# Optimization experiments

Hardware: AMD Instinct MI355X
Metric: run time of the kernel (lower is better)

The kernel has to match this reference:

```python
import jax, jax.numpy as jnp
import numpy as np

CHUNK = 6  # SmoothLoss chunk length hard-coded in TotalLoss.forward


def setup_inputs() -> dict:
    key = jax.random.key(0)
    k1, k2, k3, k4, k5 = jax.random.split(key, 5)
    N = 3_000_000   # gru/resnet/y length, divisible by 6
    M = 500_000     # one average per 6-sample chunk
    return {
        "resnet_pred": jax.random.normal(k1, (N,), dtype=jnp.float32),
        "gru_pred": jax.random.normal(k2, (N,), dtype=jnp.float32),
        "average_pred": jax.random.normal(k3, (M,), dtype=jnp.float32),
        "y": jax.random.normal(k4, (N,), dtype=jnp.float32),
        "average_hr": jax.random.normal(k5, (M,), dtype=jnp.float32),
    }


def reference(resnet_pred, gru_pred, average_pred, y, average_hr):
    lambda_val = 100.0
    # L1 losses (mean reduction, as nn.L1Loss default)
    l1_loss = jnp.mean(jnp.abs(resnet_pred - y)) + jnp.mean(jnp.abs(average_pred - average_hr))
    # Smoothness loss: for each chunk of 6, sum_t |x_t - mean(chunk)| / 6, summed over chunks
    x = gru_pred.reshape(-1, CHUNK)                      # [C, 6]
    m = jnp.mean(x, axis=1, keepdims=True)               # [C, 1]
    smooth_loss = jnp.sum(jnp.abs(x - m)) / CHUNK        # scalar
    total_loss = l1_loss + lambda_val * smooth_loss
    return (total_loss, l1_loss, smooth_loss)
```

## Files before the change

kernel.cpp:

```cpp
#include <hip/hip_runtime.h>

#define CHUNK 6
#define BLK 256

__global__ __launch_bounds__(BLK) void loss_partial_kernel(
    const float* __restrict__ resnet, const float* __restrict__ gru,
    const float* __restrict__ avgp,   const float* __restrict__ y,
    const float* __restrict__ avgh,
    float* __restrict__ partials, int nb, int C, int M, int N)
{
    const int tid = threadIdx.x;
    const int gid = blockIdx.x * BLK + tid;
    const int T   = nb * BLK;

    float s_l1a = 0.f, s_l1b = 0.f, s_sm = 0.f;

    const int Cq = C >> 2;
    const float4* g4 = reinterpret_cast<const float4*>(gru);
    float4 q0, q1, q2, q3, q4, q5;
    const bool have_q = (gid < Cq);
    if (have_q) {
        const float4* p = g4 + 6 * gid;
        q0 = p[0]; q1 = p[1]; q2 = p[2]; q3 = p[3]; q4 = p[4]; q5 = p[5];
    }

    const int Mv4 = M >> 2;
    if (gid < Mv4) {
        float4 p = reinterpret_cast<const float4*>(avgp)[gid];
        float4 h = reinterpret_cast<const float4*>(avgh)[gid];
        s_l1b = fabsf(p.x - h.x) + fabsf(p.y - h.y)
              + fabsf(p.z - h.z) + fabsf(p.w - h.w);
    }

    const int Nv4 = N >> 2;
    const float4* r4 = reinterpret_cast<const float4*>(resnet);
    const float4* y4 = reinterpret_cast<const float4*>(y);
    for (int i = gid; i < Nv4; i += T) {
        float4 r = r4[i], v = y4[i];
        s_l1a += fabsf(r.x - v.x) + fabsf(r.y - v.y)
               + fabsf(r.z - v.z) + fabsf(r.w - v.w);
    }

    if (have_q) {
        float m0 = (q0.x + q0.y + q0.z + q0.w + q1.x + q1.y) * (1.0f / 6.0f);
        float m1 = (q1.z + q1.w + q2.x + q2.y + q2.z + q2.w) * (1.0f / 6.0f);
        float m2 = (q3.x + q3.y + q3.z + q3.w + q4.x + q4.y) * (1.0f / 6.0f);
        float m3 = (q4.z + q4.w + q5.x + q5.y + q5.z + q5.w) * (1.0f / 6.0f);
        s_sm = fabsf(q0.x-m0)+fabsf(q0.y-m0)+fabsf(q0.z-m0)+fabsf(q0.w-m0)
             + fabsf(q1.x-m0)+fabsf(q1.y-m0)
             + fabsf(q1.z-m1)+fabsf(q1.w-m1)
             + fabsf(q2.x-m1)+fabsf(q2.y-m1)+fabsf(q2.z-m1)+fabsf(q2.w-m1)
             + fabsf(q3.x-m2)+fabsf(q3.y-m2)+fabsf(q3.z-m2)+fabsf(q3.w-m2)
             + fabsf(q4.x-m2)+fabsf(q4.y-m2)
             + fabsf(q4.z-m3)+fabsf(q4.w-m3)
             + fabsf(q5.x-m3)+fabsf(q5.y-m3)+fabsf(q5.z-m3)+fabsf(q5.w-m3);
    }

    if (gid == 0) {
        for (int k = Nv4 << 2; k < N; ++k) s_l1a += fabsf(resnet[k] - y[k]);
        for (int k = Mv4 << 2; k < M; ++k) s_l1b += fabsf(avgp[k] - avgh[k]);
        for (int c = Cq << 2; c < C; ++c) {
            int base = CHUNK * c;
            float x0=gru[base],x1=gru[base+1],x2=gru[base+2];
            float x3=gru[base+3],x4=gru[base+4],x5=gru[base+5];
            float m = (x0+x1+x2+x3+x4+x5) * (1.0f/6.0f);
            s_sm += fabsf(x0-m)+fabsf(x1-m)+fabsf(x2-m)
                  + fabsf(x3-m)+fabsf(x4-m)+fabsf(x5-m);
        }
    }

    #pragma unroll
    for (int off = 32; off > 0; off >>= 1) {
        s_l1a += __shfl_down(s_l1a, off, 64);
        s_l1b += __shfl_down(s_l1b, off, 64);
        s_sm  += __shfl_down(s_sm,  off, 64);
    }
    __shared__ float red0[4], red1[4], red2[4];
    int wave = tid >> 6, lane = tid & 63;
    if (lane == 0) { red0[wave] = s_l1a; red1[wave] = s_l1b; red2[wave] = s_sm; }
    __syncthreads();

    if (tid == 0) {
        partials[blockIdx.x]          = red0[0] + red0[1] + red0[2] + red0[3];
        partials[nb + blockIdx.x]     = red1[0] + red1[1] + red1[2] + red1[3];
        partials[2 * nb + blockIdx.x] = red2[0] + red2[1] + red2[2] + red2[3];
    }
}

__global__ __launch_bounds__(256) void loss_reduce_kernel(
    const float* __restrict__ partials, int nb,
    float* __restrict__ out, int N, int M)
{
    double a = 0.0, b = 0.0, c = 0.0;
    for (int i = threadIdx.x; i < nb; i += 256) {
        a += (double)partials[i];
        b += (double)partials[nb + i];
        c += (double)partials[2 * nb + i];
    }
    #pragma unroll
    for (int off = 32; off > 0; off >>= 1) {
        a += __shfl_down(a, off, 64);
        b += __shfl_down(b, off, 64);
        c += __shfl_down(c, off, 64);
    }
    __shared__ double ra[4], rb[4], rc[4];
    int wave = threadIdx.x >> 6, lane = threadIdx.x & 63;
    if (lane == 0) { ra[wave] = a; rb[wave] = b; rc[wave] = c; }
    __syncthreads();

    if (threadIdx.x == 0) {
        double sa = ra[0] + ra[1] + ra[2] + ra[3];
        double sb = rb[0] + rb[1] + rb[2] + rb[3];
        double sc = rc[0] + rc[1] + rc[2] + rc[3];
        double l1     = sa / (double)N + sb / (double)M;
        double smooth = sc / (double)CHUNK;
        double total  = l1 + 100.0 * smooth;
        out[0] = (float)total;
        out[1] = (float)l1;
        out[2] = (float)smooth;
    }
}

extern "C" void kernel_launch(void* const* d_in, const int* in_sizes, int n_in,
                              void* d_out, int out_size, void* d_ws, size_t ws_size,
                              hipStream_t stream) {
    const float* resnet = (const float*)d_in[0];
    const float* gru    = (const float*)d_in[1];
    const float* avgp   = (const float*)d_in[2];
    const float* y      = (const float*)d_in[3];
    const float* avgh   = (const float*)d_in[4];
    float* out = (float*)d_out;

    int N = in_sizes[0];
    int M = in_sizes[2];
    int C = N / CHUNK;

    int Cq  = C >> 2;
    int Mv4 = M >> 2;
    int work = (Cq > Mv4) ? Cq : Mv4;
    if (work < 1) work = 1;
    int nb = (work + BLK - 1) / BLK;

    float* partials = (float*)d_ws;

    loss_partial_kernel<<<nb, BLK, 0, stream>>>(resnet, gru, avgp, y, avgh,
                                                partials, nb, C, M, N);
    loss_reduce_kernel<<<1, 256, 0, stream>>>(partials, nb, out, N, M);
}
```

Before: 13.57 us.

## Coalesce GRU smoothness loads with wave-shuffle chunk means and grid-stride loops

Each lane now loads one contiguous float4 of the GRU input, and pairs of 6-element chunks are reconstructed across groups of three lanes using wave shuffles. This replaces the old scheme where each thread loaded six strided float4s, which gave poorly coalesced 96-byte-per-thread accesses. The average-pred L1 term also becomes a grid-stride loop. In exchange, one lane in 64 sits idle, some shuffle and select instructions are added, and a grid-stride loop now runs over the GRU data instead of a single pass.

```diff
diff --git a/kernel.cpp b/kernel.cpp
--- a/kernel.cpp
+++ b/kernel.cpp
@@ -9,27 +9,21 @@
     const float* __restrict__ avgh,
     float* __restrict__ partials, int nb, int C, int M, int N)
 {
-    const int tid = threadIdx.x;
-    const int gid = blockIdx.x * BLK + tid;
-    const int T   = nb * BLK;
+    const int tid  = threadIdx.x;
+    const int gid  = blockIdx.x * BLK + tid;
+    const int T    = nb * BLK;
+    const int lane = tid & 63;
+    const int wv0  = (blockIdx.x * (BLK >> 6)) + (tid >> 6);
+    const int NW   = nb * (BLK >> 6);
 
     float s_l1a = 0.f, s_l1b = 0.f, s_sm = 0.f;
 
-    const int Cq = C >> 2;
-    const float4* g4 = reinterpret_cast<const float4*>(gru);
-    float4 q0, q1, q2, q3, q4, q5;
-    const bool have_q = (gid < Cq);
-    if (have_q) {
-        const float4* p = g4 + 6 * gid;
-        q0 = p[0]; q1 = p[1]; q2 = p[2]; q3 = p[3]; q4 = p[4]; q5 = p[5];
-    }
-
     const int Mv4 = M >> 2;
-    if (gid < Mv4) {
-        float4 p = reinterpret_cast<const float4*>(avgp)[gid];
-        float4 h = reinterpret_cast<const float4*>(avgh)[gid];
-        s_l1b = fabsf(p.x - h.x) + fabsf(p.y - h.y)
-              + fabsf(p.z - h.z) + fabsf(p.w - h.w);
+    for (int i = gid; i < Mv4; i += T) {
+        float4 p = reinterpret_cast<const float4*>(avgp)[i];
+        float4 h = reinterpret_cast<const float4*>(avgh)[i];
+        s_l1b += fabsf(p.x - h.x) + fabsf(p.y - h.y)
+               + fabsf(p.z - h.z) + fabsf(p.w - h.w);
     }
 
     const int Nv4 = N >> 2;
@@ -41,26 +35,39 @@
                + fabsf(r.z - v.z) + fabsf(r.w - v.w);
     }
 
-    if (have_q) {
-        float m0 = (q0.x + q0.y + q0.z + q0.w + q1.x + q1.y) * (1.0f / 6.0f);
-        float m1 = (q1.z + q1.w + q2.x + q2.y + q2.z + q2.w) * (1.0f / 6.0f);
-        float m2 = (q3.x + q3.y + q3.z + q3.w + q4.x + q4.y) * (1.0f / 6.0f);
-        float m3 = (q4.z + q4.w + q5.x + q5.y + q5.z + q5.w) * (1.0f / 6.0f);
-        s_sm = fabsf(q0.x-m0)+fabsf(q0.y-m0)+fabsf(q0.z-m0)+fabsf(q0.w-m0)
-             + fabsf(q1.x-m0)+fabsf(q1.y-m0)
-             + fabsf(q1.z-m1)+fabsf(q1.w-m1)
-             + fabsf(q2.x-m1)+fabsf(q2.y-m1)+fabsf(q2.z-m1)+fabsf(q2.w-m1)
-             + fabsf(q3.x-m2)+fabsf(q3.y-m2)+fabsf(q3.z-m2)+fabsf(q3.w-m2)
-             + fabsf(q4.x-m2)+fabsf(q4.y-m2)
-             + fabsf(q4.z-m3)+fabsf(q4.w-m3)
-             + fabsf(q5.x-m3)+fabsf(q5.y-m3)+fabsf(q5.z-m3)+fabsf(q5.w-m3);
+    {
+        const int G3 = 3 * (C >> 1);
+        const float4* g4 = reinterpret_cast<const float4*>(gru);
+        const float inv6 = 1.0f / 6.0f;
+        const int r = lane % 3;
+        for (int base = wv0 * 63; base < G3; base += NW * 63) {
+            const int idx = base + lane;
+            float4 v = make_float4(0.f, 0.f, 0.f, 0.f);
+            const bool act = (lane < 63) && (idx < G3);
+            if (act) v = g4[idx];
+            const float s   = v.x + v.y + v.z + v.w;
+            const float hlo = v.x + v.y;
+            const float hhi = v.z + v.w;
+            const float v1 = (r == 0) ? s : hhi;
+            const float v2 = (r == 1) ? hlo : s;
+            const float recv1 = __shfl(v1, lane - 1, 64);
+            const float recv2 = __shfl(v2, lane + 1, 64);
+            if (act) {
+                float mA = (r == 0) ? (s + recv2) * inv6
+                         : (r == 1) ? (recv1 + hlo) * inv6
+                                    : (recv1 + s) * inv6;
+                float mB = (r == 1) ? (hhi + recv2) * inv6 : mA;
+                s_sm += fabsf(v.x - mA) + fabsf(v.y - mA)
+                      + fabsf(v.z - mB) + fabsf(v.w - mB);
+            }
+        }
     }
 
     if (gid == 0) {
         for (int k = Nv4 << 2; k < N; ++k) s_l1a += fabsf(resnet[k] - y[k]);
         for (int k = Mv4 << 2; k < M; ++k) s_l1b += fabsf(avgp[k] - avgh[k]);
-        for (int c = Cq << 2; c < C; ++c) {
-            int base = CHUNK * c;
+        if (C & 1) {
+            int base = CHUNK * (C - 1);
             float x0=gru[base],x1=gru[base+1],x2=gru[base+2];
             float x3=gru[base+3],x4=gru[base+4],x5=gru[base+5];
             float m = (x0+x1+x2+x3+x4+x5) * (1.0f/6.0f);
@@ -76,7 +83,7 @@
         s_sm  += __shfl_down(s_sm,  off, 64);
     }
     __shared__ float red0[4], red1[4], red2[4];
-    int wave = tid >> 6, lane = tid & 63;
+    int wave = tid >> 6;
     if (lane == 0) { red0[wave] = s_l1a; red1[wave] = s_l1b; red2[wave] = s_sm; }
     __syncthreads();
 
```

After: 15.35 us. 1.13x slower.
